# Kernel tuning notes

Hardware: AMD Instinct MI355X
Metric: run time of the kernel (lower is better)

## Reference

```python
import jax, jax.numpy as jnp
import numpy as np

POOL = 2  # pooling_size == pooling_stride == 2, SAME padding, H even -> no actual pad


def setup_inputs() -> dict:
    key = jax.random.key(0)
    k1, k2 = jax.random.split(key)
    B, H, C = 8, 28, 32
    mu_in = jax.random.normal(k1, (B, H, H, C), dtype=jnp.float32)
    # per-channel spatial covariance: [B, H*H, H*H, C]
    Sigma_in = jax.random.uniform(k2, (B, H * H, H * H, C), dtype=jnp.float32)
    return {"mu_in": mu_in, "Sigma_in": Sigma_in}


def reference(mu_in, Sigma_in):
    B, H, W, C = mu_in.shape
    ho, wo = H // POOL, W // POOL
    # non-overlapping 2x2 windows, row-major within window (matches TF argmax order)
    patches = mu_in.reshape(B, ho, POOL, wo, POOL, C).transpose(0, 1, 3, 2, 4, 5)
    patches = patches.reshape(B, ho, wo, POOL * POOL, C)
    mu_out = jnp.max(patches, axis=3)                     # [B, ho, wo, C]
    k = jnp.argmax(patches, axis=3)                       # [B, ho, wo, C], first-match ties like TF
    dy, dx = k // POOL, k % POOL
    iy = POOL * jnp.arange(ho)[None, :, None, None] + dy  # input row of the max
    ix = POOL * jnp.arange(wo)[None, None, :, None] + dx  # input col of the max
    # TF decode: index = y*hw_in + x  (flat spatial index in the input image)
    index = (iy * W + ix).astype(jnp.int32)               # [B, ho, wo, C]
    index = index.transpose(0, 3, 1, 2).reshape(B, C, ho * wo)  # [B, C, N_out]
    # Sigma: [B, N_in, N_in, C] -> [B, C, N_in, N_in], then double gather
    S1 = Sigma_in.transpose(0, 3, 1, 2)
    g1 = jnp.take_along_axis(S1, index[:, :, :, None], axis=2)       # [B, C, N_out, N_in]
    Sigma_out = jnp.take_along_axis(g1, index[:, :, None, :], axis=3)  # [B, C, N_out, N_out]
    Sigma_out = Sigma_out.transpose(0, 2, 3, 1)           # [B, N_out, N_out, C]
    return mu_out, Sigma_out
```

## Files before the change

kernel.cpp:

```cpp
#include <hip/hip_runtime.h>
#include <stdint.h>

#define BATCH 8
#define HIN   28
#define CH    32
#define HO    14
#define NIN   784
#define NOUT  196

#define NITEM  (4 * NIN * 8)
#define ITERS  (NITEM / 256)
#define UNROLL 7
#define OUTER  (ITERS / UNROLL)
#define TILE_W (NOUT * CH)

typedef float f32x4 __attribute__((ext_vector_type(4)));

__global__ __launch_bounds__(256, 4) void vdp_pool_fused_kernel(
        const float* __restrict__ mu_in,
        const float* __restrict__ sigma_in,
        float* __restrict__ mu_out,
        float* __restrict__ sigma_out)
{
    __shared__ __align__(16) float out_tile[TILE_W + 64];
    __shared__ uint32_t colmask[NOUT * 8];
    __shared__ uint32_t cmq[NIN * 2];

    const int blk = blockIdx.x;
    const int b   = blk / NOUT;
    const int p   = blk - b * NOUT;
    const int tid = threadIdx.x;

    for (int w = tid; w < NOUT * 2; w += 256) {
        const int q2   = w >> 1;
        const int half = w & 1;
        const int qy = q2 / HO, qx = q2 - qy * HO;
        const float* base =
            mu_in + (((size_t)b * HIN + 2 * qy) * HIN + 2 * qx) * CH + half * 16;

        uint32_t kqh = 0;
        #pragma unroll
        for (int g = 0; g < 4; ++g) {
            const float4 v0 = *(const float4*)(base + g * 4);
            const float4 v1 = *(const float4*)(base + CH + g * 4);
            const float4 v2 = *(const float4*)(base + HIN * CH + g * 4);
            const float4 v3 = *(const float4*)(base + HIN * CH + CH + g * 4);
            float m0, m1, m2, m3;
            uint32_t k0, k1, k2, k3;
            { float best = v0.x; uint32_t k = 0;
              if (v1.x > best) { best = v1.x; k = 1; }
              if (v2.x > best) { best = v2.x; k = 2; }
              if (v3.x > best) { best = v3.x; k = 3; }
              m0 = best; k0 = k; }
            { float best = v0.y; uint32_t k = 0;
              if (v1.y > best) { best = v1.y; k = 1; }
              if (v2.y > best) { best = v2.y; k = 2; }
              if (v3.y > best) { best = v3.y; k = 3; }
              m1 = best; k1 = k; }
            { float best = v0.z; uint32_t k = 0;
              if (v1.z > best) { best = v1.z; k = 1; }
              if (v2.z > best) { best = v2.z; k = 2; }
              if (v3.z > best) { best = v3.z; k = 3; }
              m2 = best; k2 = k; }
            { float best = v0.w; uint32_t k = 0;
              if (v1.w > best) { best = v1.w; k = 1; }
              if (v2.w > best) { best = v2.w; k = 2; }
              if (v3.w > best) { best = v3.w; k = 3; }
              m3 = best; k3 = k; }
            kqh |= (k0 << (2 * (g * 4 + 0))) | (k1 << (2 * (g * 4 + 1))) |
                   (k2 << (2 * (g * 4 + 2))) | (k3 << (2 * (g * 4 + 3)));
            if (q2 == p) {
                *(float4*)(mu_out + (size_t)blk * CH + half * 16 + g * 4) =
                    make_float4(m0, m1, m2, m3);
            }
        }
        #pragma unroll
        for (int dj = 0; dj < 4; ++dj) {
            uint32_t m = 0;
            #pragma unroll
            for (int cl = 0; cl < 16; ++cl)
                m |= (((kqh >> (2 * cl)) & 3u) == (uint32_t)dj) ? (1u << cl) : 0u;
            colmask[q2 * 8 + dj * 2 + half] = m;
        }
    }
    __syncthreads();

    for (int j = tid; j < NIN; j += 256) {
        const int jy = j / HIN, jx = j - jy * HIN;
        const int q  = (jy >> 1) * HO + (jx >> 1);
        const int dj = ((jy & 1) << 1) | (jx & 1);
        const uint32_t qb = (uint32_t)(q * CH) << 16;
        cmq[j * 2 + 0] = qb | colmask[q * 8 + dj * 2 + 0];
        cmq[j * 2 + 1] = qb | colmask[q * 8 + dj * 2 + 1];
    }
    const uint32_t half = ((uint32_t)tid >> 2) & 1u;
    const uint32_t shs  = ((uint32_t)tid & 3u) * 4u;
    const uint32_t hs   = half * 16u + shs;
    unsigned long long rmpack = 0ull;
    #pragma unroll
    for (int r = 0; r < 4; ++r)
        rmpack |= (unsigned long long)(colmask[p * 8 + r * 2 + (int)half] & 0xFFFFu)
                  << (16 * r);
    __syncthreads();

    const float* sb = sigma_in + (size_t)b * NIN * NIN * CH;
    const int py = p / HO, px = p - py * HO;
    const uint32_t ibase = (uint32_t)(2 * py) * HIN + 2u * px;
    const uint32_t rjb   = (uint32_t)tid >> 3;
    const uint32_t trash = TILE_W + ((uint32_t)tid & 63u);

    for (int o = 0; o < OUTER; ++o) {
        f32x4    val[UNROLL];
        uint32_t tab[UNROLL];
        uint32_t rmv[UNROLL];
        #pragma unroll
        for (int u = 0; u < UNROLL; ++u) {
            const uint32_t rj = rjb + (uint32_t)(o * UNROLL + u) * 32u;
            const uint32_t r  = rj / NIN;
            const uint32_t j  = rj - r * NIN;
            const uint32_t i  = ibase + (r >> 1) * HIN + (r & 1u);
            val[u] = __builtin_nontemporal_load(
                (const f32x4*)(sb + (((size_t)i * NIN + j) << 5) + hs));
            tab[u] = cmq[j * 2 + half];
            rmv[u] = (uint32_t)(rmpack >> (r * 16u)) & 0xFFFFu;
        }
        #pragma unroll
        for (int u = 0; u < UNROLL; ++u) {
            const uint32_t sel16 = rmv[u] & (tab[u] & 0xFFFFu);
            const uint32_t s4    = (sel16 >> shs) & 0xFu;
            const uint32_t base  = (tab[u] >> 16) + hs;
            out_tile[(s4 & 1u) ? base + 0u : trash] = val[u][0];
            out_tile[(s4 & 2u) ? base + 1u : trash] = val[u][1];
            out_tile[(s4 & 4u) ? base + 2u : trash] = val[u][2];
            out_tile[(s4 & 8u) ? base + 3u : trash] = val[u][3];
        }
    }
    __syncthreads();

    {
        const f32x4* srcT = (const f32x4*)out_tile;
        f32x4* dstT = (f32x4*)(sigma_out + (size_t)blk * TILE_W);
        for (int w = tid; w < TILE_W / 4; w += 256)
            __builtin_nontemporal_store(srcT[w], &dstT[w]);
    }
}

extern "C" void kernel_launch(void* const* d_in, const int* in_sizes, int n_in,
                              void* d_out, int out_size, void* d_ws, size_t ws_size,
                              hipStream_t stream) {
    const float* mu_in    = (const float*)d_in[0];
    const float* sigma_in = (const float*)d_in[1];

    float* mu_out    = (float*)d_out;
    float* sigma_out = (float*)d_out + BATCH * NOUT * CH;

    vdp_pool_fused_kernel<<<BATCH * NOUT, 256, 0, stream>>>(
        mu_in, sigma_in, mu_out, sigma_out);
}
```

Baseline: 135.0 us.

## Skip sigma loads for unselected rows, drop colmask LDS, prefetch tables

Each thread now redirects its sigma load to a fixed dummy address whenever none of its 16 channels (the 32-channel half it belongs to) is selected by the row/column argmax masks. This cuts most of the scattered HBM traffic, since only about a quarter of column positions per channel are kept. The change also writes cmq directly from the pooling pass, removing the colmask array, one LDS pass and one barrier. It prefetches the next iteration's cmq table entries into registers and raises the launch-bounds occupancy hint from 4 to 5. The dummy loads still issue instructions and hit the same address, and the higher occupancy target may constrain register allocation.

```diff
diff --git a/kernel.cpp b/kernel.cpp
--- a/kernel.cpp
+++ b/kernel.cpp
@@ -16,14 +16,13 @@
 
 typedef float f32x4 __attribute__((ext_vector_type(4)));
 
-__global__ __launch_bounds__(256, 4) void vdp_pool_fused_kernel(
+__global__ __launch_bounds__(256, 5) void vdp_pool_fused_kernel(
         const float* __restrict__ mu_in,
         const float* __restrict__ sigma_in,
         float* __restrict__ mu_out,
         float* __restrict__ sigma_out)
 {
     __shared__ __align__(16) float out_tile[TILE_W + 64];
-    __shared__ uint32_t colmask[NOUT * 8];
     __shared__ uint32_t cmq[NIN * 2];
 
     const int blk = blockIdx.x;
@@ -33,10 +32,10 @@
 
     for (int w = tid; w < NOUT * 2; w += 256) {
         const int q2   = w >> 1;
-        const int half = w & 1;
+        const int hf   = w & 1;
         const int qy = q2 / HO, qx = q2 - qy * HO;
         const float* base =
-            mu_in + (((size_t)b * HIN + 2 * qy) * HIN + 2 * qx) * CH + half * 16;
+            mu_in + (((size_t)b * HIN + 2 * qy) * HIN + 2 * qx) * CH + hf * 16;
 
         uint32_t kqh = 0;
         #pragma unroll
@@ -70,69 +69,84 @@
             kqh |= (k0 << (2 * (g * 4 + 0))) | (k1 << (2 * (g * 4 + 1))) |
                    (k2 << (2 * (g * 4 + 2))) | (k3 << (2 * (g * 4 + 3)));
             if (q2 == p) {
-                *(float4*)(mu_out + (size_t)blk * CH + half * 16 + g * 4) =
+                *(float4*)(mu_out + (size_t)blk * CH + hf * 16 + g * 4) =
                     make_float4(m0, m1, m2, m3);
             }
         }
+        const uint32_t qb = (uint32_t)(q2 * CH) << 16;
+        const uint32_t jb = (uint32_t)(2 * qy) * HIN + 2u * qx;
         #pragma unroll
         for (int dj = 0; dj < 4; ++dj) {
             uint32_t m = 0;
             #pragma unroll
             for (int cl = 0; cl < 16; ++cl)
                 m |= (((kqh >> (2 * cl)) & 3u) == (uint32_t)dj) ? (1u << cl) : 0u;
-            colmask[q2 * 8 + dj * 2 + half] = m;
+            const uint32_t j = jb + (uint32_t)(dj >> 1) * HIN + (dj & 1);
+            cmq[j * 2 + hf] = qb | m;
         }
     }
     __syncthreads();
 
-    for (int j = tid; j < NIN; j += 256) {
-        const int jy = j / HIN, jx = j - jy * HIN;
-        const int q  = (jy >> 1) * HO + (jx >> 1);
-        const int dj = ((jy & 1) << 1) | (jx & 1);
-        const uint32_t qb = (uint32_t)(q * CH) << 16;
-        cmq[j * 2 + 0] = qb | colmask[q * 8 + dj * 2 + 0];
-        cmq[j * 2 + 1] = qb | colmask[q * 8 + dj * 2 + 1];
-    }
     const uint32_t half = ((uint32_t)tid >> 2) & 1u;
     const uint32_t shs  = ((uint32_t)tid & 3u) * 4u;
     const uint32_t hs   = half * 16u + shs;
+    const int py = p / HO, px = p - py * HO;
+    const uint32_t ibase = (uint32_t)(2 * py) * HIN + 2u * px;
+
     unsigned long long rmpack = 0ull;
     #pragma unroll
-    for (int r = 0; r < 4; ++r)
-        rmpack |= (unsigned long long)(colmask[p * 8 + r * 2 + (int)half] & 0xFFFFu)
-                  << (16 * r);
-    __syncthreads();
+    for (int r = 0; r < 4; ++r) {
+        const uint32_t jp = ibase + (uint32_t)(r >> 1) * HIN + (r & 1);
+        rmpack |= (unsigned long long)(cmq[jp * 2 + half] & 0xFFFFu) << (16 * r);
+    }
 
     const float* sb = sigma_in + (size_t)b * NIN * NIN * CH;
-    const int py = p / HO, px = p - py * HO;
-    const uint32_t ibase = (uint32_t)(2 * py) * HIN + 2u * px;
     const uint32_t rjb   = (uint32_t)tid >> 3;
     const uint32_t trash = TILE_W + ((uint32_t)tid & 63u);
 
+    uint32_t tab[UNROLL];
+    #pragma unroll
+    for (int u = 0; u < UNROLL; ++u) {
+        const uint32_t rj = rjb + (uint32_t)u * 32u;
+        const uint32_t r  = rj / NIN;
+        const uint32_t j  = rj - r * NIN;
+        tab[u] = cmq[j * 2 + half];
+    }
+
     for (int o = 0; o < OUTER; ++o) {
         f32x4    val[UNROLL];
-        uint32_t tab[UNROLL];
-        uint32_t rmv[UNROLL];
+        uint32_t off[UNROLL];
+        uint32_t s4p[UNROLL];
         #pragma unroll
         for (int u = 0; u < UNROLL; ++u) {
             const uint32_t rj = rjb + (uint32_t)(o * UNROLL + u) * 32u;
             const uint32_t r  = rj / NIN;
             const uint32_t j  = rj - r * NIN;
             const uint32_t i  = ibase + (r >> 1) * HIN + (r & 1u);
+            const uint32_t sel16 =
+                ((uint32_t)(rmpack >> (r * 16u)) & tab[u]) & 0xFFFFu;
+            const float* a = sb + (((size_t)i * NIN + j) << 5) + hs;
             val[u] = __builtin_nontemporal_load(
-                (const f32x4*)(sb + (((size_t)i * NIN + j) << 5) + hs));
-            tab[u] = cmq[j * 2 + half];
-            rmv[u] = (uint32_t)(rmpack >> (r * 16u)) & 0xFFFFu;
+                (const f32x4*)(sel16 ? a : (sb + hs)));
+            off[u] = (tab[u] >> 16) + hs;
+            s4p[u] = (sel16 >> shs) & 0xFu;
+        }
+        if (o + 1 < OUTER) {
+            #pragma unroll
+            for (int u = 0; u < UNROLL; ++u) {
+                const uint32_t rj = rjb + (uint32_t)((o + 1) * UNROLL + u) * 32u;
+                const uint32_t r  = rj / NIN;
+                const uint32_t j  = rj - r * NIN;
+                tab[u] = cmq[j * 2 + half];
+            }
         }
         #pragma unroll
         for (int u = 0; u < UNROLL; ++u) {
-            const uint32_t sel16 = rmv[u] & (tab[u] & 0xFFFFu);
-            const uint32_t s4    = (sel16 >> shs) & 0xFu;
-            const uint32_t base  = (tab[u] >> 16) + hs;
-            out_tile[(s4 & 1u) ? base + 0u : trash] = val[u][0];
-            out_tile[(s4 & 2u) ? base + 1u : trash] = val[u][1];
-            out_tile[(s4 & 4u) ? base + 2u : trash] = val[u][2];
-            out_tile[(s4 & 8u) ? base + 3u : trash] = val[u][3];
+            const uint32_t s4 = s4p[u], bs = off[u];
+            out_tile[(s4 & 1u) ? bs + 0u : trash] = val[u][0];
+            out_tile[(s4 & 2u) ? bs + 1u : trash] = val[u][1];
+            out_tile[(s4 & 4u) ? bs + 2u : trash] = val[u][2];
+            out_tile[(s4 & 8u) ? bs + 3u : trash] = val[u][3];
         }
     }
     __syncthreads();
```

New measurement: 138.3 us. +2.5%, slower.

## Remap blocks across XCDs, write cmq directly, swizzle LDS tile, use cached loads

Applied to the files above, without the earlier changes.

Blocks are remapped so that consecutive output positions p on the same XCD share a contiguous range, which is meant to improve L2 locality of the sigma rows each XCD reads. The colmask staging array and its second pass and barrier are removed, with cmq written directly during the argmax phase. The per-iteration position mapping changes so each wave walks contiguous positions. LDS writes use a per-row rotation swizzle to cut bank conflicts, undone on readout. Sigma loads switch from nontemporal to normal cached loads, which risks extra cache pollution.

```diff
diff --git a/kernel.cpp b/kernel.cpp
--- a/kernel.cpp
+++ b/kernel.cpp
@@ -8,10 +8,10 @@
 #define NIN   784
 #define NOUT  196
 
-#define NITEM  (4 * NIN * 8)
-#define ITERS  (NITEM / 256)
+#define NPOS   (4 * NIN)
+#define WPI    224
 #define UNROLL 7
-#define OUTER  (ITERS / UNROLL)
+#define OUTER  (NPOS / WPI)
 #define TILE_W (NOUT * CH)
 
 typedef float f32x4 __attribute__((ext_vector_type(4)));
@@ -23,20 +23,22 @@
         float* __restrict__ sigma_out)
 {
     __shared__ __align__(16) float out_tile[TILE_W + 64];
-    __shared__ uint32_t colmask[NOUT * 8];
     __shared__ uint32_t cmq[NIN * 2];
 
     const int blk = blockIdx.x;
     const int b   = blk / NOUT;
-    const int p   = blk - b * NOUT;
+    const int o2  = blk - b * NOUT;
+    const int xcd = o2 & 7;
+    const int m   = o2 >> 3;
+    const int p   = (xcd < 4) ? xcd * 25 + m : 100 + (xcd - 4) * 24 + m;
     const int tid = threadIdx.x;
 
     for (int w = tid; w < NOUT * 2; w += 256) {
         const int q2   = w >> 1;
-        const int half = w & 1;
+        const int hf   = w & 1;
         const int qy = q2 / HO, qx = q2 - qy * HO;
         const float* base =
-            mu_in + (((size_t)b * HIN + 2 * qy) * HIN + 2 * qx) * CH + half * 16;
+            mu_in + (((size_t)b * HIN + 2 * qy) * HIN + 2 * qx) * CH + hf * 16;
 
         uint32_t kqh = 0;
         #pragma unroll
@@ -70,43 +72,40 @@
             kqh |= (k0 << (2 * (g * 4 + 0))) | (k1 << (2 * (g * 4 + 1))) |
                    (k2 << (2 * (g * 4 + 2))) | (k3 << (2 * (g * 4 + 3)));
             if (q2 == p) {
-                *(float4*)(mu_out + (size_t)blk * CH + half * 16 + g * 4) =
+                *(float4*)(mu_out + ((size_t)b * NOUT + p) * CH + hf * 16 + g * 4) =
                     make_float4(m0, m1, m2, m3);
             }
         }
+        const uint32_t qb = (uint32_t)(q2 * CH) << 16;
+        const uint32_t jb = (uint32_t)(2 * qy) * HIN + 2u * qx;
         #pragma unroll
         for (int dj = 0; dj < 4; ++dj) {
-            uint32_t m = 0;
+            uint32_t mm = 0;
             #pragma unroll
             for (int cl = 0; cl < 16; ++cl)
-                m |= (((kqh >> (2 * cl)) & 3u) == (uint32_t)dj) ? (1u << cl) : 0u;
-            colmask[q2 * 8 + dj * 2 + half] = m;
+                mm |= (((kqh >> (2 * cl)) & 3u) == (uint32_t)dj) ? (1u << cl) : 0u;
+            const uint32_t j = jb + (uint32_t)(dj >> 1) * HIN + (dj & 1);
+            cmq[j * 2 + hf] = qb | mm;
         }
     }
     __syncthreads();
 
-    for (int j = tid; j < NIN; j += 256) {
-        const int jy = j / HIN, jx = j - jy * HIN;
-        const int q  = (jy >> 1) * HO + (jx >> 1);
-        const int dj = ((jy & 1) << 1) | (jx & 1);
-        const uint32_t qb = (uint32_t)(q * CH) << 16;
-        cmq[j * 2 + 0] = qb | colmask[q * 8 + dj * 2 + 0];
-        cmq[j * 2 + 1] = qb | colmask[q * 8 + dj * 2 + 1];
-    }
-    const uint32_t half = ((uint32_t)tid >> 2) & 1u;
-    const uint32_t shs  = ((uint32_t)tid & 3u) * 4u;
-    const uint32_t hs   = half * 16u + shs;
+    const uint32_t itm  = (uint32_t)tid & 7u;
+    const uint32_t hs   = itm * 4u;
+    const uint32_t half = itm >> 2;
+    const uint32_t shs  = (itm & 3u) * 4u;
+    const uint32_t posb = ((uint32_t)tid >> 6) * 56u + (((uint32_t)tid >> 3) & 7u);
+    const int py = p / HO, px = p - py * HO;
+    const uint32_t ibase = (uint32_t)(2 * py) * HIN + 2u * px;
+
     unsigned long long rmpack = 0ull;
     #pragma unroll
-    for (int r = 0; r < 4; ++r)
-        rmpack |= (unsigned long long)(colmask[p * 8 + r * 2 + (int)half] & 0xFFFFu)
-                  << (16 * r);
-    __syncthreads();
+    for (int r = 0; r < 4; ++r) {
+        const uint32_t jp = ibase + (uint32_t)(r >> 1) * HIN + (r & 1);
+        rmpack |= (unsigned long long)(cmq[jp * 2 + half] & 0xFFFFu) << (16 * r);
+    }
 
     const float* sb = sigma_in + (size_t)b * NIN * NIN * CH;
-    const int py = p / HO, px = p - py * HO;
-    const uint32_t ibase = (uint32_t)(2 * py) * HIN + 2u * px;
-    const uint32_t rjb   = (uint32_t)tid >> 3;
     const uint32_t trash = TILE_W + ((uint32_t)tid & 63u);
 
     for (int o = 0; o < OUTER; ++o) {
@@ -115,12 +114,11 @@
         uint32_t rmv[UNROLL];
         #pragma unroll
         for (int u = 0; u < UNROLL; ++u) {
-            const uint32_t rj = rjb + (uint32_t)(o * UNROLL + u) * 32u;
-            const uint32_t r  = rj / NIN;
-            const uint32_t j  = rj - r * NIN;
-            const uint32_t i  = ibase + (r >> 1) * HIN + (r & 1u);
-            val[u] = __builtin_nontemporal_load(
-                (const f32x4*)(sb + (((size_t)i * NIN + j) << 5) + hs));
+            const uint32_t pos = (uint32_t)o * WPI + (uint32_t)u * 8u + posb;
+            const uint32_t r   = pos / NIN;
+            const uint32_t j   = pos - r * NIN;
+            const uint32_t i   = ibase + (r >> 1) * HIN + (r & 1u);
+            val[u] = *(const f32x4*)(sb + (((size_t)i * NIN + j) << 5) + hs);
             tab[u] = cmq[j * 2 + half];
             rmv[u] = (uint32_t)(rmpack >> (r * 16u)) & 0xFFFFu;
         }
@@ -128,20 +126,27 @@
         for (int u = 0; u < UNROLL; ++u) {
             const uint32_t sel16 = rmv[u] & (tab[u] & 0xFFFFu);
             const uint32_t s4    = (sel16 >> shs) & 0xFu;
-            const uint32_t base  = (tab[u] >> 16) + hs;
-            out_tile[(s4 & 1u) ? base + 0u : trash] = val[u][0];
-            out_tile[(s4 & 2u) ? base + 1u : trash] = val[u][1];
-            out_tile[(s4 & 4u) ? base + 2u : trash] = val[u][2];
-            out_tile[(s4 & 8u) ? base + 3u : trash] = val[u][3];
+            const uint32_t qb    = tab[u] >> 16;
+            const uint32_t rot   = (qb >> 3) & 31u;
+            const uint32_t base0 = qb + ((hs + rot) & 31u);
+            out_tile[(s4 & 1u) ? qb + ((hs + 0u + rot) & 31u) : trash] = val[u][0];
+            out_tile[(s4 & 2u) ? qb + ((hs + 1u + rot) & 31u) : trash] = val[u][1];
+            out_tile[(s4 & 4u) ? qb + ((hs + 2u + rot) & 31u) : trash] = val[u][2];
+            out_tile[(s4 & 8u) ? qb + ((hs + 3u + rot) & 31u) : trash] = val[u][3];
+            (void)base0;
         }
     }
     __syncthreads();
 
     {
-        const f32x4* srcT = (const f32x4*)out_tile;
-        f32x4* dstT = (f32x4*)(sigma_out + (size_t)blk * TILE_W);
-        for (int w = tid; w < TILE_W / 4; w += 256)
-            __builtin_nontemporal_store(srcT[w], &dstT[w]);
+        f32x4* dstT = (f32x4*)(sigma_out + ((size_t)b * NOUT + p) * TILE_W);
+        for (int w = tid; w < TILE_W / 4; w += 256) {
+            const uint32_t q   = (uint32_t)w >> 3;
+            const uint32_t v   = ((uint32_t)w & 7u) * 4u;
+            const uint32_t rot = (q * 4u) & 31u;
+            const f32x4 x = *(const f32x4*)(out_tile + q * 32u + ((v + rot) & 31u));
+            __builtin_nontemporal_store(x, &dstT[w]);
+        }
     }
 }
 
```

After: 146.8 us. 1.09x slower.
